# Performance work log

Hardware: AMD Instinct MI355X
Metric: run time of the kernel (lower is better)

## Reference

```python
import jax, jax.numpy as jnp
import numpy as np

K, D, O, B = 65536, 256, 256, 1024

def setup_inputs() -> dict:
    key = jax.random.key(0)
    k1, k2, k3 = jax.random.split(key, 3)
    return {
        "x": jax.random.normal(k1, (B, D), dtype=jnp.float32),
        "mean": jax.random.normal(k2, (K, D), dtype=jnp.float32),
        "stddev": jnp.ones((K, D), dtype=jnp.float32),
        "outputs": jax.random.normal(k3, (K, O), dtype=jnp.float32),
        "top_k": 32,
    }

def reference(x, mean, stddev, outputs, top_k):
    # Joint Gaussian log-prob summed over feature dim, computed without the
    # [B, K, D] broadcast torch materializes. Expanding sum_d ((x-mu)/sigma)^2
    # gives three GEMM-shaped terms.
    d = x.shape[-1]
    inv_var = 1.0 / (stddev * stddev)                      # [K, D]
    quad = ((x * x) @ inv_var.T                            # [B, K]
            - 2.0 * (x @ (mean * inv_var).T)
            + jnp.sum(mean * mean * inv_var, axis=-1))
    log_norm = jnp.sum(jnp.log(stddev), axis=-1) + 0.5 * d * jnp.log(2.0 * jnp.pi)
    joint_lp = -0.5 * quad - log_norm                      # [B, K]
    top_lp, top_idx = jax.lax.top_k(joint_lp, top_k)       # [B, top_k]
    weights = jax.nn.softmax(top_lp, axis=-1)              # [B, top_k]
    gathered = outputs[top_idx]                            # [B, top_k, O]
    return jnp.einsum('bko,bk->bo', gathered, weights)     # [B, O]
```

## Files before the change

### kernel.cpp

```cpp
#include <hip/hip_runtime.h>
#include <stdint.h>

#define KCOMP 65536
#define DDIM  256
#define ODIM  256
#define BROWS 1024
#define NCB   1024
#define LOG2PI_TERM 235.2482645f

typedef float f32x4 __attribute__((ext_vector_type(4)));
typedef __bf16 bf16x8 __attribute__((ext_vector_type(8)));
typedef unsigned int u32;
typedef unsigned long long u64;
typedef unsigned short u16;

typedef __attribute__((address_space(1))) const u32 gconst_u32;
typedef __attribute__((address_space(3))) u32 lds_u32;

__device__ __forceinline__ u16 f2bf(float f) {
  u32 b = __float_as_uint(f);
  b += 0x7FFFu + ((b >> 16) & 1u);
  return (u16)(b >> 16);
}
__device__ __forceinline__ u32 fkey(float f) {
  u32 b = __float_as_uint(f);
  return b ^ ((b >> 31) ? 0xFFFFFFFFu : 0x80000000u);
}

#define DPP_ROR1 0x121
#define DPP_ROR2 0x122
#define DPP_ROR4 0x124
#define DPP_ROR8 0x128

#define WS_A     0
#define WS_KEY   (1u << 20)

__global__ void prep_A(const float* __restrict__ x, u16* __restrict__ A) {
  int l = threadIdx.x & 63;
  int wv = threadIdx.x >> 6;
  int t = blockIdx.x;
  int row = t * 16 + (l & 15);
  for (int u = 0; u < 4; ++u) {
    int cc = wv * 4 + u;
    int d0 = cc * 16 + ((l >> 4) << 2);
    float4 xv = *(const float4*)(x + (size_t)row * DDIM + d0);
    float xs[4] = {xv.x, xv.y, xv.z, xv.w};
    uint4 v;
    u32 wds[4];
    for (int e = 0; e < 4; ++e)
      wds[e] = (u32)f2bf(xs[e] * xs[e]) | ((u32)f2bf(-2.0f * xs[e]) << 16);
    v.x = wds[0]; v.y = wds[1]; v.z = wds[2]; v.w = wds[3];
    *(uint4*)(A + ((size_t)(t * 16 + cc) * 64 + l) * 8) = v;
  }
}

__global__ __launch_bounds__(512, 4)
void main_gemm(const u16* __restrict__ A_ws, const float* __restrict__ mean,
               const float* __restrict__ stdd, u32* __restrict__ ckey) {
  __shared__ __align__(16) char lds_raw[66560];
  __shared__ u32 wsel[2][32][9];
  int tid = threadIdx.x, l = tid & 63, w = tid >> 6;
  int nb = blockIdx.x;
  int p = l & 15, q = l >> 4;
  int rt = w >> 2;
  int cg = w & 3;

  u32 kid0 = (u32)(cg * 16 + q * 4);

  bf16x8 wf[16];
  float myc0;
  f32x4 mycv;
  {
    u32* scr = (u32*)(lds_raw + w * 8320);
    int p8 = l & 7, q8 = l >> 3;
#pragma unroll
    for (int rr = 0; rr < 2; ++rr) {
      int comp = (nb * 4 + cg) * 16 + rr * 8 + p8;
      const float* mrow = mean + (size_t)comp * DDIM + q8 * 32;
      const float* srow = stdd + (size_t)comp * DDIM + q8 * 32;
      float gsum = 0.f;
#pragma unroll
      for (int i = 0; i < 8; ++i) {
        float4 m4 = *(const float4*)(mrow + 4 * i);
        float4 s4 = *(const float4*)(srow + 4 * i);
        float ms[4] = {m4.x, m4.y, m4.z, m4.w};
        float ss[4] = {s4.x, s4.y, s4.z, s4.w};
        u32 wd[4];
#pragma unroll
        for (int e = 0; e < 4; ++e) {
          float iv = __builtin_amdgcn_rcpf(ss[e] * ss[e]);
          float miv = ms[e] * iv;
          wd[e] = (u32)f2bf(-0.5f * iv) | ((u32)f2bf(-0.5f * miv) << 16);
          gsum -= 0.5f * ms[e] * miv + __logf(ss[e]);
        }
        uint4 v; v.x = wd[0]; v.y = wd[1]; v.z = wd[2]; v.w = wd[3];
        *(uint4*)(scr + p8 * 260 + q8 * 32 + i * 4) = v;
      }
      gsum += __shfl_xor(gsum, 8);
      gsum += __shfl_xor(gsum, 16);
      gsum += __shfl_xor(gsum, 32);
      if ((p >> 3) == rr) {
        myc0 = gsum - LOG2PI_TERM;
#pragma unroll
        for (int cc = 0; cc < 16; ++cc)
          wf[cc] = *(const bf16x8*)(scr + (p & 7) * 260 + cc * 16 + q * 4);
      }
    }
#pragma unroll
    for (int i = 0; i < 4; ++i)
      mycv[i] = __shfl(myc0, q * 4 + i);
  }
  __syncthreads();

#define ASHP(B, CELL) (lds_raw + ((size_t)(B) * 32 + (CELL)) * 1024)

#define ISSUE(S, B)                                                           \
  {                                                                           \
    _Pragma("unroll")                                                         \
    for (int u = 0; u < 4; ++u) {                                             \
      int cell = w * 4 + u;                                                   \
      const u16* gsrc = A_ws +                                                \
        ((size_t)((S) * 2 + (cell >> 4)) * 16 + (cell & 15)) * 512            \
        + (size_t)l * 8;                                                      \
      __builtin_amdgcn_global_load_lds((gconst_u32*)gsrc,                     \
          (lds_u32*)ASHP(B, cell), 16, 0, 0);                                 \
    }                                                                         \
  }

#define MERGE_EMIT(ST, B)                                                     \
  {                                                                           \
    int r = tid;                                                              \
    u32 b1 = ~0u, b2 = ~0u;                                                   \
    _Pragma("unroll")                                                         \
    for (int j = 0; j < 8; ++j) {                                             \
      u32 key = wsel[B][r][j];                                                \
      if (key < b1) { b2 = b1; b1 = key; }                                    \
      else if (key < b2) { b2 = key; }                                        \
    }                                                                         \
    int rowg = (ST) * 32 + r;                                                 \
    uint2 ov; ov.x = ~b1; ov.y = ~b2;                                         \
    *(uint2*)&ckey[((size_t)rowg * NCB + nb) * 2] = ov;                       \
  }

  ISSUE(0, 0)
  for (int s = 0; s < 32; ++s) {
    int pb = s & 1;
    __syncthreads();
    if (s < 31) ISSUE(s + 1, pb ^ 1)
    if (s > 0 && tid < 32) MERGE_EMIT(s - 1, pb ^ 1)

    f32x4 aca = mycv;
    f32x4 acb = (f32x4){0.f, 0.f, 0.f, 0.f};
    __builtin_amdgcn_s_setprio(1);
#pragma unroll
    for (int cc = 0; cc < 8; ++cc) {
      bf16x8 a0 = *(const bf16x8*)(ASHP(pb, rt * 16 + cc) + (size_t)l * 16);
      bf16x8 a1 = *(const bf16x8*)(ASHP(pb, rt * 16 + 8 + cc) + (size_t)l * 16);
      aca = __builtin_amdgcn_mfma_f32_16x16x32_bf16(wf[cc], a0, aca, 0, 0, 0);
      acb = __builtin_amdgcn_mfma_f32_16x16x32_bf16(wf[8 + cc], a1, acb, 0, 0, 0);
    }
    __builtin_amdgcn_s_setprio(0);
    f32x4 ac;
    ac[0] = aca[0] + acb[0]; ac[1] = aca[1] + acb[1];
    ac[2] = aca[2] + acb[2]; ac[3] = aca[3] + acb[3];

#define UMIN(a, b) ((a) < (b) ? (a) : (b))
#define UMAX(a, b) ((a) < (b) ? (b) : (a))
    {
      u32 k0 = (__float_as_uint(ac[0]) & 0xFFFFFF00u) | (kid0 + 0);
      u32 k1 = (__float_as_uint(ac[1]) & 0xFFFFFF00u) | (kid0 + 1);
      u32 k2 = (__float_as_uint(ac[2]) & 0xFFFFFF00u) | (kid0 + 2);
      u32 k3 = (__float_as_uint(ac[3]) & 0xFFFFFF00u) | (kid0 + 3);
      u32 l0 = UMIN(k0, k1), h0 = UMAX(k0, k1);
      u32 l1 = UMIN(k2, k3), h1 = UMAX(k2, k3);
      u32 m1 = UMIN(l0, l1), m2 = UMIN(UMAX(l0, l1), UMIN(h0, h1));
      {
        u32 o1 = (u32)__shfl_xor((int)m1, 16);
        u32 o2 = (u32)__shfl_xor((int)m2, 16);
        u32 lo = UMIN(m1, o1), hi = UMAX(m1, o1), mn = UMIN(m2, o2);
        m1 = lo; m2 = UMIN(hi, mn);
      }
      {
        u32 o1 = (u32)__shfl_xor((int)m1, 32);
        u32 o2 = (u32)__shfl_xor((int)m2, 32);
        u32 lo = UMIN(m1, o1), hi = UMAX(m1, o1), mn = UMIN(m2, o2);
        m1 = lo; m2 = UMIN(hi, mn);
      }
      if (q == 0) {
        int r = rt * 16 + p;
        wsel[pb][r][cg * 2] = m1;
        wsel[pb][r][cg * 2 + 1] = m2;
      }
    }
#undef UMIN
#undef UMAX
  }
  __syncthreads();
  if (tid < 32) MERGE_EMIT(31, 1)
#undef ISSUE
#undef MERGE_EMIT
#undef ASHP
}

__global__ __launch_bounds__(256)
void finalize(const float* __restrict__ x, const float* __restrict__ mean,
              const float* __restrict__ stdd, const float* __restrict__ outs,
              const u32* __restrict__ ckey, float* __restrict__ out) {
  __shared__ u32 cksh[2048];
  __shared__ float xr[256];
  __shared__ float part[256];
  __shared__ int selk[64];
  __shared__ float ew[32];
  __shared__ int kf[32];
  __shared__ float invs_sh;
  int tid = threadIdx.x, l = tid & 63, v = tid >> 6;
  int row = blockIdx.x;

  for (int i = tid; i < 2048; i += 256)
    cksh[i] = ckey[(size_t)row * 2048 + i];
  xr[tid] = x[(size_t)row * DDIM + tid];
  __syncthreads();

#define REDUCE_MAX(m)                                                         \
  {                                                                           \
    u32 o;                                                                    \
    o = (u32)__builtin_amdgcn_mov_dpp((int)m, DPP_ROR1, 0xf, 0xf, false);     \
    m = m > o ? m : o;                                                        \
    o = (u32)__builtin_amdgcn_mov_dpp((int)m, DPP_ROR2, 0xf, 0xf, false);     \
    m = m > o ? m : o;                                                        \
    o = (u32)__builtin_amdgcn_mov_dpp((int)m, DPP_ROR4, 0xf, 0xf, false);     \
    m = m > o ? m : o;                                                        \
    o = (u32)__builtin_amdgcn_mov_dpp((int)m, DPP_ROR8, 0xf, 0xf, false);     \
    m = m > o ? m : o;                                                        \
    o = (u32)__shfl_xor((int)m, 16); m = m > o ? m : o;                       \
    o = (u32)__shfl_xor((int)m, 32); m = m > o ? m : o;                       \
  }

  {
    u32 ext[8];
#pragma unroll
    for (int i = 0; i < 8; ++i) {
      int j = v * 512 + i * 64 + l;
      ext[i] = (cksh[j] & 0xFFFFFE00u) | ((u32)l << 3) | (u32)i;
    }
#define CSW(a, b) { if (ext[a] < ext[b]) { u32 t = ext[a]; ext[a] = ext[b]; ext[b] = t; } }
    CSW(0,1) CSW(2,3) CSW(4,5) CSW(6,7)
    CSW(0,2) CSW(1,3) CSW(4,6) CSW(5,7)
    CSW(1,2) CSW(5,6)
    CSW(0,4) CSW(1,5) CSW(2,6) CSW(3,7)
    CSW(2,4) CSW(3,5)
    CSW(1,2) CSW(3,4) CSW(5,6)
#undef CSW
    for (int it = 0; it < 16; ++it) {
      u32 m = ext[0];
      REDUCE_MAX(m)
      if (m == ext[0]) {
#pragma unroll
        for (int z = 0; z < 7; ++z) ext[z] = ext[z + 1];
        ext[7] = 0;
      }
      if (l == 0) {
        int wl = (int)((m >> 3) & 63u), wi = (int)(m & 7u);
        int j = v * 512 + wi * 64 + wl;
        selk[v * 16 + it] = (int)((u32)(j >> 1) * 64u + (~cksh[j] & 0x3Fu));
      }
    }
  }
  __syncthreads();

  {
    int j = tid >> 2, qq = tid & 3;
    int k = selk[j];
    const float* mr = mean + (size_t)k * DDIM + qq * 64;
    const float* sr = stdd + (size_t)k * DDIM + qq * 64;
    float s2 = 0.f, ls = 0.f;
    for (int i = 0; i < 16; ++i) {
      float4 m4 = *(const float4*)(mr + 4 * i);
      float4 s4 = *(const float4*)(sr + 4 * i);
      float4 x4 = *(const float4*)(&xr[qq * 64 + 4 * i]);
      { float is = __builtin_amdgcn_rcpf(s4.x); float df = (x4.x - m4.x) * is; s2 += df * df; ls += __logf(s4.x); }
      { float is = __builtin_amdgcn_rcpf(s4.y); float df = (x4.y - m4.y) * is; s2 += df * df; ls += __logf(s4.y); }
      { float is = __builtin_amdgcn_rcpf(s4.z); float df = (x4.z - m4.z) * is; s2 += df * df; ls += __logf(s4.z); }
      { float is = __builtin_amdgcn_rcpf(s4.w); float df = (x4.w - m4.w) * is; s2 += df * df; ls += __logf(s4.w); }
    }
    part[tid] = -0.5f * s2 - ls;
  }
  __syncthreads();

  if (tid < 64) {
    float lp0 = part[l * 4] + part[l * 4 + 1] + part[l * 4 + 2] +
                part[l * 4 + 3] - LOG2PI_TERM;
    u32 ext = (fkey(lp0) & 0xFFFFFFC0u) | (u32)l;
    float maxlp = 0.f, ssum = 0.f;
    for (int it = 0; it < 32; ++it) {
      u32 m = ext;
      REDUCE_MAX(m)
      int j = (int)(m & 63u);
      u32 vb = m & 0xFFFFFFC0u;
      vb ^= (vb >> 31) ? 0x80000000u : 0xFFFFFFFFu;
      float lp = __uint_as_float(vb);
      if (it == 0) maxlp = lp;
      float e = __expf(lp - maxlp);
      ssum += e;
      if (l == 0) { ew[it] = e; kf[it] = selk[j]; }
      if (j == l) ext = 0;
    }
    if (l == 0) invs_sh = 1.0f / ssum;
  }
  __syncthreads();
#undef REDUCE_MAX

  {
    float a = 0.f;
    for (int i = 0; i < 32; ++i)
      a += ew[i] * outs[(size_t)kf[i] * ODIM + tid];
    out[(size_t)row * ODIM + tid] = a * invs_sh;
  }
}

extern "C" void kernel_launch(void* const* d_in, const int* in_sizes, int n_in,
                              void* d_out, int out_size, void* d_ws, size_t ws_size,
                              hipStream_t stream) {
  const float* x = (const float*)d_in[0];
  const float* mean = (const float*)d_in[1];
  const float* stdd = (const float*)d_in[2];
  const float* outs = (const float*)d_in[3];
  char* ws = (char*)d_ws;
  u16* A_ws = (u16*)(ws + WS_A);
  u32* ckey = (u32*)(ws + WS_KEY);

  prep_A<<<64, 256, 0, stream>>>(x, A_ws);
  main_gemm<<<NCB, 512, 0, stream>>>(A_ws, mean, stdd, ckey);
  finalize<<<BROWS, 256, 0, stream>>>(x, mean, stdd, outs, ckey,
                                      (float*)d_out);
}
```

Measured before the change: 338.8 us.

## Precompute bf16 weight tiles in a separate pass and retile GEMM for larger component blocks

```diff
diff --git a/kernel.cpp b/kernel.cpp
--- a/kernel.cpp
+++ b/kernel.cpp
@@ -5,7 +5,6 @@
 #define DDIM  256
 #define ODIM  256
 #define BROWS 1024
-#define NCB   1024
 #define LOG2PI_TERM 235.2482645f
 
 typedef float f32x4 __attribute__((ext_vector_type(4)));
@@ -32,8 +31,27 @@
 #define DPP_ROR4 0x124
 #define DPP_ROR8 0x128
 
-#define WS_A     0
-#define WS_KEY   (1u << 20)
+#define WS_A      0u
+#define WS_W      (1u << 20)
+#define WS_MYC    (65u << 20)
+#define WS_KEYB   ((65u << 20) + (1u << 18))
+#define WS_NEED_BIG ((size_t)WS_KEYB + (4u << 20))
+#define WS_KEYS   (1u << 20)
+
+#define REDUCE_MAX(m)                                                         \
+  {                                                                           \
+    u32 o;                                                                    \
+    o = (u32)__builtin_amdgcn_mov_dpp((int)m, DPP_ROR1, 0xf, 0xf, false);     \
+    m = m > o ? m : o;                                                        \
+    o = (u32)__builtin_amdgcn_mov_dpp((int)m, DPP_ROR2, 0xf, 0xf, false);     \
+    m = m > o ? m : o;                                                        \
+    o = (u32)__builtin_amdgcn_mov_dpp((int)m, DPP_ROR4, 0xf, 0xf, false);     \
+    m = m > o ? m : o;                                                        \
+    o = (u32)__builtin_amdgcn_mov_dpp((int)m, DPP_ROR8, 0xf, 0xf, false);     \
+    m = m > o ? m : o;                                                        \
+    o = (u32)__shfl_xor((int)m, 16); m = m > o ? m : o;                       \
+    o = (u32)__shfl_xor((int)m, 32); m = m > o ? m : o;                       \
+  }
 
 __global__ void prep_A(const float* __restrict__ x, u16* __restrict__ A) {
   int l = threadIdx.x & 63;
@@ -54,73 +72,66 @@
   }
 }
 
+__global__ void prep_W(const float* __restrict__ mean,
+                       const float* __restrict__ stdd,
+                       u16* __restrict__ W, float* __restrict__ myc) {
+  __shared__ float psum[4][16];
+  int l = threadIdx.x & 63;
+  int wv = threadIdx.x >> 6;
+  int t = blockIdx.x;
+  int comp = t * 16 + (l & 15);
+  float gsum = 0.f;
+  for (int u = 0; u < 4; ++u) {
+    int cc = wv * 4 + u;
+    int d0 = cc * 16 + ((l >> 4) << 2);
+    float4 m4 = *(const float4*)(mean + (size_t)comp * DDIM + d0);
+    float4 s4 = *(const float4*)(stdd + (size_t)comp * DDIM + d0);
+    float ms[4] = {m4.x, m4.y, m4.z, m4.w};
+    float ss[4] = {s4.x, s4.y, s4.z, s4.w};
+    uint4 v;
+    u32 wds[4];
+    for (int e = 0; e < 4; ++e) {
+      float iv = __builtin_amdgcn_rcpf(ss[e] * ss[e]);
+      float miv = ms[e] * iv;
+      wds[e] = (u32)f2bf(-0.5f * iv) | ((u32)f2bf(-0.5f * miv) << 16);
+      gsum -= 0.5f * ms[e] * miv + __logf(ss[e]);
+    }
+    v.x = wds[0]; v.y = wds[1]; v.z = wds[2]; v.w = wds[3];
+    *(uint4*)(W + ((size_t)(t * 16 + cc) * 64 + l) * 8) = v;
+  }
+  gsum += __shfl_xor(gsum, 16);
+  gsum += __shfl_xor(gsum, 32);
+  if (l < 16) psum[wv][l] = gsum;
+  __syncthreads();
+  if (threadIdx.x < 16)
+    myc[t * 16 + threadIdx.x] = psum[0][threadIdx.x] + psum[1][threadIdx.x] +
+                                psum[2][threadIdx.x] + psum[3][threadIdx.x] -
+                                LOG2PI_TERM;
+}
+
 __global__ __launch_bounds__(512, 4)
-void main_gemm(const u16* __restrict__ A_ws, const float* __restrict__ mean,
-               const float* __restrict__ stdd, u32* __restrict__ ckey) {
-  __shared__ __align__(16) char lds_raw[66560];
-  __shared__ u32 wsel[2][32][9];
+void main_gemm_big(const u16* __restrict__ A_ws, const u16* __restrict__ W_ws,
+                   const float* __restrict__ myc_ws, u32* __restrict__ ckey) {
+  __shared__ __align__(16) char Ash[2][32][1024];
+  __shared__ u32 wsel[2][32][17];
   int tid = threadIdx.x, l = tid & 63, w = tid >> 6;
   int nb = blockIdx.x;
+  int nbc = nb & 127;
+  int rs = nb >> 7;
   int p = l & 15, q = l >> 4;
-  int rt = w >> 2;
-  int cg = w & 3;
-
-  u32 kid0 = (u32)(cg * 16 + q * 4);
-
-  bf16x8 wf[16];
-  float myc0;
-  f32x4 mycv;
-  {
-    u32* scr = (u32*)(lds_raw + w * 8320);
-    int p8 = l & 7, q8 = l >> 3;
-#pragma unroll
-    for (int rr = 0; rr < 2; ++rr) {
-      int comp = (nb * 4 + cg) * 16 + rr * 8 + p8;
-      const float* mrow = mean + (size_t)comp * DDIM + q8 * 32;
-      const float* srow = stdd + (size_t)comp * DDIM + q8 * 32;
-      float gsum = 0.f;
-#pragma unroll
-      for (int i = 0; i < 8; ++i) {
-        float4 m4 = *(const float4*)(mrow + 4 * i);
-        float4 s4 = *(const float4*)(srow + 4 * i);
-        float ms[4] = {m4.x, m4.y, m4.z, m4.w};
-        float ss[4] = {s4.x, s4.y, s4.z, s4.w};
-        u32 wd[4];
-#pragma unroll
-        for (int e = 0; e < 4; ++e) {
-          float iv = __builtin_amdgcn_rcpf(ss[e] * ss[e]);
-          float miv = ms[e] * iv;
-          wd[e] = (u32)f2bf(-0.5f * iv) | ((u32)f2bf(-0.5f * miv) << 16);
-          gsum -= 0.5f * ms[e] * miv + __logf(ss[e]);
-        }
-        uint4 v; v.x = wd[0]; v.y = wd[1]; v.z = wd[2]; v.w = wd[3];
-        *(uint4*)(scr + p8 * 260 + q8 * 32 + i * 4) = v;
-      }
-      gsum += __shfl_xor(gsum, 8);
-      gsum += __shfl_xor(gsum, 16);
-      gsum += __shfl_xor(gsum, 32);
-      if ((p >> 3) == rr) {
-        myc0 = gsum - LOG2PI_TERM;
-#pragma unroll
-        for (int cc = 0; cc < 16; ++cc)
-          wf[cc] = *(const bf16x8*)(scr + (p & 7) * 260 + cc * 16 + q * 4);
-      }
-    }
-#pragma unroll
-    for (int i = 0; i < 4; ++i)
-      mycv[i] = __shfl(myc0, q * 4 + i);
-  }
-  __syncthreads();
-
-#define ASHP(B, CELL) (lds_raw + ((size_t)(B) * 32 + (CELL)) * 1024)
-
+
+  int Cb = nbc * 512 + w * 64;
+  u32 kid0 = (u32)(w * 64 + q * 4);
+  const u16* Wl = W_ws + (size_t)(Cb >> 4) * 16 * 512 + (size_t)l * 8;
+
+#define ASHP(B, CELL) (&Ash[B][CELL][0])
 #define ISSUE(S, B)                                                           \
   {                                                                           \
     _Pragma("unroll")                                                         \
     for (int u = 0; u < 4; ++u) {                                             \
       int cell = w * 4 + u;                                                   \
       const u16* gsrc = A_ws +                                                \
-        ((size_t)((S) * 2 + (cell >> 4)) * 16 + (cell & 15)) * 512            \
+        ((size_t)((rs * 16 + (S) * 2 + (cell >> 4)) * 16) + (cell & 15)) * 512\
         + (size_t)l * 8;                                                      \
       __builtin_amdgcn_global_load_lds((gconst_u32*)gsrc,                     \
           (lds_u32*)ASHP(B, cell), 16, 0, 0);                                 \
@@ -130,50 +141,82 @@
 #define MERGE_EMIT(ST, B)                                                     \
   {                                                                           \
     int r = tid;                                                              \
-    u32 b1 = ~0u, b2 = ~0u;                                                   \
+    u32 top[8] = {~0u, ~0u, ~0u, ~0u, ~0u, ~0u, ~0u, ~0u};                    \
     _Pragma("unroll")                                                         \
-    for (int j = 0; j < 8; ++j) {                                             \
+    for (int j = 0; j < 16; ++j) {                                            \
       u32 key = wsel[B][r][j];                                                \
-      if (key < b1) { b2 = b1; b1 = key; }                                    \
-      else if (key < b2) { b2 = key; }                                        \
+      if (key < top[7]) {                                                     \
+        top[7] = key;                                                         \
+        for (int z = 7; z > 0 && top[z] < top[z - 1]; --z) {                  \
+          u32 tt = top[z]; top[z] = top[z - 1]; top[z - 1] = tt;              \
+        }                                                                     \
+      }                                                                       \
     }                                                                         \
-    int rowg = (ST) * 32 + r;                                                 \
-    uint2 ov; ov.x = ~b1; ov.y = ~b2;                                         \
-    *(uint2*)&ckey[((size_t)rowg * NCB + nb) * 2] = ov;                       \
+    int rowg = rs * 256 + (ST) * 32 + r;                                      \
+    size_t base = ((size_t)rowg * 128 + nbc) * 8;                             \
+    uint4 o1; o1.x = ~top[0]; o1.y = ~top[1]; o1.z = ~top[2]; o1.w = ~top[3]; \
+    uint4 o2; o2.x = ~top[4]; o2.y = ~top[5]; o2.z = ~top[6]; o2.w = ~top[7]; \
+    *(uint4*)&ckey[base] = o1;                                                \
+    *(uint4*)&ckey[base + 4] = o2;                                            \
   }
 
   ISSUE(0, 0)
-  for (int s = 0; s < 32; ++s) {
+  for (int s = 0; s < 8; ++s) {
     int pb = s & 1;
     __syncthreads();
-    if (s < 31) ISSUE(s + 1, pb ^ 1)
+    if (s < 7) ISSUE(s + 1, pb ^ 1)
     if (s > 0 && tid < 32) MERGE_EMIT(s - 1, pb ^ 1)
 
-    f32x4 aca = mycv;
-    f32x4 acb = (f32x4){0.f, 0.f, 0.f, 0.f};
+    f32x4 acc[2][4];
+#pragma unroll
+    for (int ct = 0; ct < 4; ++ct) {
+      f32x4 mv = *(const f32x4*)(myc_ws + Cb + ct * 16 + q * 4);
+      acc[0][ct] = mv;
+      acc[1][ct] = mv;
+    }
     __builtin_amdgcn_s_setprio(1);
 #pragma unroll
-    for (int cc = 0; cc < 8; ++cc) {
-      bf16x8 a0 = *(const bf16x8*)(ASHP(pb, rt * 16 + cc) + (size_t)l * 16);
-      bf16x8 a1 = *(const bf16x8*)(ASHP(pb, rt * 16 + 8 + cc) + (size_t)l * 16);
-      aca = __builtin_amdgcn_mfma_f32_16x16x32_bf16(wf[cc], a0, aca, 0, 0, 0);
-      acb = __builtin_amdgcn_mfma_f32_16x16x32_bf16(wf[8 + cc], a1, acb, 0, 0, 0);
+    for (int cc = 0; cc < 16; ++cc) {
+      bf16x8 a0 = *(const bf16x8*)(ASHP(pb, cc) + (size_t)l * 16);
+      bf16x8 a1 = *(const bf16x8*)(ASHP(pb, 16 + cc) + (size_t)l * 16);
+      bf16x8 w0 = *(const bf16x8*)(Wl + (size_t)(0 * 16 + cc) * 512);
+      bf16x8 w1 = *(const bf16x8*)(Wl + (size_t)(1 * 16 + cc) * 512);
+      bf16x8 w2 = *(const bf16x8*)(Wl + (size_t)(2 * 16 + cc) * 512);
+      bf16x8 w3 = *(const bf16x8*)(Wl + (size_t)(3 * 16 + cc) * 512);
+      acc[0][0] = __builtin_amdgcn_mfma_f32_16x16x32_bf16(w0, a0, acc[0][0], 0, 0, 0);
+      acc[1][0] = __builtin_amdgcn_mfma_f32_16x16x32_bf16(w0, a1, acc[1][0], 0, 0, 0);
+      acc[0][1] = __builtin_amdgcn_mfma_f32_16x16x32_bf16(w1, a0, acc[0][1], 0, 0, 0);
+      acc[1][1] = __builtin_amdgcn_mfma_f32_16x16x32_bf16(w1, a1, acc[1][1], 0, 0, 0);
+      acc[0][2] = __builtin_amdgcn_mfma_f32_16x16x32_bf16(w2, a0, acc[0][2], 0, 0, 0);
+      acc[1][2] = __builtin_amdgcn_mfma_f32_16x16x32_bf16(w2, a1, acc[1][2], 0, 0, 0);
+      acc[0][3] = __builtin_amdgcn_mfma_f32_16x16x32_bf16(w3, a0, acc[0][3], 0, 0, 0);
+      acc[1][3] = __builtin_amdgcn_mfma_f32_16x16x32_bf16(w3, a1, acc[1][3], 0, 0, 0);
     }
     __builtin_amdgcn_s_setprio(0);
-    f32x4 ac;
-    ac[0] = aca[0] + acb[0]; ac[1] = aca[1] + acb[1];
-    ac[2] = aca[2] + acb[2]; ac[3] = aca[3] + acb[3];
 
 #define UMIN(a, b) ((a) < (b) ? (a) : (b))
 #define UMAX(a, b) ((a) < (b) ? (b) : (a))
-    {
-      u32 k0 = (__float_as_uint(ac[0]) & 0xFFFFFF00u) | (kid0 + 0);
-      u32 k1 = (__float_as_uint(ac[1]) & 0xFFFFFF00u) | (kid0 + 1);
-      u32 k2 = (__float_as_uint(ac[2]) & 0xFFFFFF00u) | (kid0 + 2);
-      u32 k3 = (__float_as_uint(ac[3]) & 0xFFFFFF00u) | (kid0 + 3);
-      u32 l0 = UMIN(k0, k1), h0 = UMAX(k0, k1);
-      u32 l1 = UMIN(k2, k3), h1 = UMAX(k2, k3);
-      u32 m1 = UMIN(l0, l1), m2 = UMIN(UMAX(l0, l1), UMIN(h0, h1));
+#pragma unroll
+    for (int rt = 0; rt < 2; ++rt) {
+      u32 s1[4], s2[4];
+#pragma unroll
+      for (int ct = 0; ct < 4; ++ct) {
+        u32 kb = kid0 + (u32)(ct * 16);
+        u32 k0 = (__float_as_uint(acc[rt][ct][0]) & 0xFFFFFE00u) | kb;
+        u32 k1 = (__float_as_uint(acc[rt][ct][1]) & 0xFFFFFE00u) | (kb + 1);
+        u32 k2 = (__float_as_uint(acc[rt][ct][2]) & 0xFFFFFE00u) | (kb + 2);
+        u32 k3 = (__float_as_uint(acc[rt][ct][3]) & 0xFFFFFE00u) | (kb + 3);
+        u32 l0 = UMIN(k0, k1), h0 = UMAX(k0, k1);
+        u32 l1 = UMIN(k2, k3), h1 = UMAX(k2, k3);
+        s1[ct] = UMIN(l0, l1);
+        s2[ct] = UMIN(UMAX(l0, l1), UMIN(h0, h1));
+      }
+      u32 a1_ = UMIN(s1[0], s1[1]);
+      u32 a2_ = UMIN(UMAX(s1[0], s1[1]), UMIN(s2[0], s2[1]));
+      u32 b1_ = UMIN(s1[2], s1[3]);
+      u32 b2_ = UMIN(UMAX(s1[2], s1[3]), UMIN(s2[2], s2[3]));
+      u32 m1 = UMIN(a1_, b1_);
+      u32 m2 = UMIN(UMAX(a1_, b1_), UMIN(a2_, b2_));
       {
         u32 o1 = (u32)__shfl_xor((int)m1, 16);
         u32 o2 = (u32)__shfl_xor((int)m2, 16);
@@ -188,25 +231,25 @@
       }
       if (q == 0) {
         int r = rt * 16 + p;
-        wsel[pb][r][cg * 2] = m1;
-        wsel[pb][r][cg * 2 + 1] = m2;
+        wsel[pb][r][w * 2] = m1;
+        wsel[pb][r][w * 2 + 1] = m2;
       }
     }
 #undef UMIN
 #undef UMAX
   }
   __syncthreads();
-  if (tid < 32) MERGE_EMIT(31, 1)
+  if (tid < 32) MERGE_EMIT(7, 1)
 #undef ISSUE
 #undef MERGE_EMIT
 #undef ASHP
 }
 
 __global__ __launch_bounds__(256)
-void finalize(const float* __restrict__ x, const float* __restrict__ mean,
-              const float* __restrict__ stdd, const float* __restrict__ outs,
-              const u32* __restrict__ ckey, float* __restrict__ out) {
-  __shared__ u32 cksh[2048];
+void finalize_big(const float* __restrict__ x, const float* __restrict__ mean,
+                  const float* __restrict__ stdd, const float* __restrict__ outs,
+                  const u32* __restrict__ ckey, float* __restrict__ out) {
+  __shared__ u32 cksh[1024];
   __shared__ float xr[256];
   __shared__ float part[256];
   __shared__ int selk[64];
@@ -216,53 +259,35 @@
   int tid = threadIdx.x, l = tid & 63, v = tid >> 6;
   int row = blockIdx.x;
 
-  for (int i = tid; i < 2048; i += 256)
-    cksh[i] = ckey[(size_t)row * 2048 + i];
+  for (int i = tid; i < 1024; i += 256)
+    cksh[i] = ckey[(size_t)row * 1024 + i];
   xr[tid] = x[(size_t)row * DDIM + tid];
   __syncthreads();
 
-#define REDUCE_MAX(m)                                                         \
-  {                                                                           \
-    u32 o;                                                                    \
-    o = (u32)__builtin_amdgcn_mov_dpp((int)m, DPP_ROR1, 0xf, 0xf, false);     \
-    m = m > o ? m : o;                                                        \
-    o = (u32)__builtin_amdgcn_mov_dpp((int)m, DPP_ROR2, 0xf, 0xf, false);     \
-    m = m > o ? m : o;                                                        \
-    o = (u32)__builtin_amdgcn_mov_dpp((int)m, DPP_ROR4, 0xf, 0xf, false);     \
-    m = m > o ? m : o;                                                        \
-    o = (u32)__builtin_amdgcn_mov_dpp((int)m, DPP_ROR8, 0xf, 0xf, false);     \
-    m = m > o ? m : o;                                                        \
-    o = (u32)__shfl_xor((int)m, 16); m = m > o ? m : o;                       \
-    o = (u32)__shfl_xor((int)m, 32); m = m > o ? m : o;                       \
-  }
-
   {
-    u32 ext[8];
-#pragma unroll
-    for (int i = 0; i < 8; ++i) {
-      int j = v * 512 + i * 64 + l;
-      ext[i] = (cksh[j] & 0xFFFFFE00u) | ((u32)l << 3) | (u32)i;
+    u32 ext[4];
+#pragma unroll
+    for (int i = 0; i < 4; ++i) {
+      int j = v * 256 + i * 64 + l;
+      ext[i] = (cksh[j] & 0xFFFFFE00u) | ((u32)l << 2) | (u32)i;
     }
 #define CSW(a, b) { if (ext[a] < ext[b]) { u32 t = ext[a]; ext[a] = ext[b]; ext[b] = t; } }
-    CSW(0,1) CSW(2,3) CSW(4,5) CSW(6,7)
-    CSW(0,2) CSW(1,3) CSW(4,6) CSW(5,7)
-    CSW(1,2) CSW(5,6)
-    CSW(0,4) CSW(1,5) CSW(2,6) CSW(3,7)
-    CSW(2,4) CSW(3,5)
-    CSW(1,2) CSW(3,4) CSW(5,6)
+    CSW(0,1) CSW(2,3)
+    CSW(0,2) CSW(1,3)
+    CSW(1,2)
 #undef CSW
     for (int it = 0; it < 16; ++it) {
       u32 m = ext[0];
       REDUCE_MAX(m)
       if (m == ext[0]) {
 #pragma unroll
-        for (int z = 0; z < 7; ++z) ext[z] = ext[z + 1];
-        ext[7] = 0;
+        for (int z = 0; z < 3; ++z) ext[z] = ext[z + 1];
+        ext[3] = 0;
       }
       if (l == 0) {
-        int wl = (int)((m >> 3) & 63u), wi = (int)(m & 7u);
-        int j = v * 512 + wi * 64 + wl;
-        selk[v * 16 + it] = (int)((u32)(j >> 1) * 64u + (~cksh[j] & 0x3Fu));
+        int wl = (int)((m >> 2) & 63u), wi = (int)(m & 3u);
+        int j = v * 256 + wi * 64 + wl;
+        selk[v * 16 + it] = (int)((u32)(j >> 3) * 512u + (~cksh[j] & 0x1FFu));
       }
     }
   }
@@ -308,7 +333,251 @@
     if (l == 0) invs_sh = 1.0f / ssum;
   }
   __syncthreads();
-#undef REDUCE_MAX
+
+  {
+    float a = 0.f;
+    for (int i = 0; i < 32; ++i)
+      a += ew[i] * outs[(size_t)kf[i] * ODIM + tid];
+    out[(size_t)row * ODIM + tid] = a * invs_sh;
+  }
+}
+
+__global__ __launch_bounds__(512, 4)
+void main_gemm_small(const u16* __restrict__ A_ws, const float* __restrict__ mean,
+                     const float* __restrict__ stdd, u32* __restrict__ ckey) {
+  __shared__ __align__(16) char lds_raw[66560];
+  __shared__ u32 wsel[2][32][9];
+  int tid = threadIdx.x, l = tid & 63, w = tid >> 6;
+  int nb = blockIdx.x;
+  int p = l & 15, q = l >> 4;
+  int rt = w >> 2;
+  int cg = w & 3;
+  u32 kid0 = (u32)(cg * 16 + q * 4);
+
+  bf16x8 wf[16];
+  float myc0;
+  f32x4 mycv;
+  {
+    u32* scr = (u32*)(lds_raw + w * 8320);
+    int p8 = l & 7, q8 = l >> 3;
+#pragma unroll
+    for (int rr = 0; rr < 2; ++rr) {
+      int comp = (nb * 4 + cg) * 16 + rr * 8 + p8;
+      const float* mrow = mean + (size_t)comp * DDIM + q8 * 32;
+      const float* srow = stdd + (size_t)comp * DDIM + q8 * 32;
+      float gsum = 0.f;
+#pragma unroll
+      for (int i = 0; i < 8; ++i) {
+        float4 m4 = *(const float4*)(mrow + 4 * i);
+        float4 s4 = *(const float4*)(srow + 4 * i);
+        float ms[4] = {m4.x, m4.y, m4.z, m4.w};
+        float ss[4] = {s4.x, s4.y, s4.z, s4.w};
+        u32 wd[4];
+#pragma unroll
+        for (int e = 0; e < 4; ++e) {
+          float iv = __builtin_amdgcn_rcpf(ss[e] * ss[e]);
+          float miv = ms[e] * iv;
+          wd[e] = (u32)f2bf(-0.5f * iv) | ((u32)f2bf(-0.5f * miv) << 16);
+          gsum -= 0.5f * ms[e] * miv + __logf(ss[e]);
+        }
+        uint4 v; v.x = wd[0]; v.y = wd[1]; v.z = wd[2]; v.w = wd[3];
+        *(uint4*)(scr + p8 * 260 + q8 * 32 + i * 4) = v;
+      }
+      gsum += __shfl_xor(gsum, 8);
+      gsum += __shfl_xor(gsum, 16);
+      gsum += __shfl_xor(gsum, 32);
+      if ((p >> 3) == rr) {
+        myc0 = gsum - LOG2PI_TERM;
+#pragma unroll
+        for (int cc = 0; cc < 16; ++cc)
+          wf[cc] = *(const bf16x8*)(scr + (p & 7) * 260 + cc * 16 + q * 4);
+      }
+    }
+#pragma unroll
+    for (int i = 0; i < 4; ++i)
+      mycv[i] = __shfl(myc0, q * 4 + i);
+  }
+  __syncthreads();
+
+#define ASHP(B, CELL) (lds_raw + ((size_t)(B) * 32 + (CELL)) * 1024)
+#define ISSUE(S, B)                                                           \
+  {                                                                           \
+    _Pragma("unroll")                                                         \
+    for (int u = 0; u < 4; ++u) {                                             \
+      int cell = w * 4 + u;                                                   \
+      const u16* gsrc = A_ws +                                                \
+        ((size_t)((S) * 2 + (cell >> 4)) * 16 + (cell & 15)) * 512            \
+        + (size_t)l * 8;                                                      \
+      __builtin_amdgcn_global_load_lds((gconst_u32*)gsrc,                     \
+          (lds_u32*)ASHP(B, cell), 16, 0, 0);                                 \
+    }                                                                         \
+  }
+#define MERGE_EMIT(ST, B)                                                     \
+  {                                                                           \
+    int r = tid;                                                              \
+    u32 b1 = ~0u, b2 = ~0u;                                                   \
+    _Pragma("unroll")                                                         \
+    for (int j = 0; j < 8; ++j) {                                             \
+      u32 key = wsel[B][r][j];                                                \
+      if (key < b1) { b2 = b1; b1 = key; }                                    \
+      else if (key < b2) { b2 = key; }                                        \
+    }                                                                         \
+    int rowg = (ST) * 32 + r;                                                 \
+    uint2 ov; ov.x = ~b1; ov.y = ~b2;                                         \
+    *(uint2*)&ckey[((size_t)rowg * 1024 + nb) * 2] = ov;                      \
+  }
+
+  ISSUE(0, 0)
+  for (int s = 0; s < 32; ++s) {
+    int pb = s & 1;
+    __syncthreads();
+    if (s < 31) ISSUE(s + 1, pb ^ 1)
+    if (s > 0 && tid < 32) MERGE_EMIT(s - 1, pb ^ 1)
+
+    f32x4 aca = mycv;
+    f32x4 acb = (f32x4){0.f, 0.f, 0.f, 0.f};
+    __builtin_amdgcn_s_setprio(1);
+#pragma unroll
+    for (int cc = 0; cc < 8; ++cc) {
+      bf16x8 a0 = *(const bf16x8*)(ASHP(pb, rt * 16 + cc) + (size_t)l * 16);
+      bf16x8 a1 = *(const bf16x8*)(ASHP(pb, rt * 16 + 8 + cc) + (size_t)l * 16);
+      aca = __builtin_amdgcn_mfma_f32_16x16x32_bf16(wf[cc], a0, aca, 0, 0, 0);
+      acb = __builtin_amdgcn_mfma_f32_16x16x32_bf16(wf[8 + cc], a1, acb, 0, 0, 0);
+    }
+    __builtin_amdgcn_s_setprio(0);
+    f32x4 ac;
+    ac[0] = aca[0] + acb[0]; ac[1] = aca[1] + acb[1];
+    ac[2] = aca[2] + acb[2]; ac[3] = aca[3] + acb[3];
+
+#define UMIN(a, b) ((a) < (b) ? (a) : (b))
+#define UMAX(a, b) ((a) < (b) ? (b) : (a))
+    {
+      u32 k0 = (__float_as_uint(ac[0]) & 0xFFFFFF00u) | (kid0 + 0);
+      u32 k1 = (__float_as_uint(ac[1]) & 0xFFFFFF00u) | (kid0 + 1);
+      u32 k2 = (__float_as_uint(ac[2]) & 0xFFFFFF00u) | (kid0 + 2);
+      u32 k3 = (__float_as_uint(ac[3]) & 0xFFFFFF00u) | (kid0 + 3);
+      u32 l0 = UMIN(k0, k1), h0 = UMAX(k0, k1);
+      u32 l1 = UMIN(k2, k3), h1 = UMAX(k2, k3);
+      u32 m1 = UMIN(l0, l1), m2 = UMIN(UMAX(l0, l1), UMIN(h0, h1));
+      {
+        u32 o1 = (u32)__shfl_xor((int)m1, 16);
+        u32 o2 = (u32)__shfl_xor((int)m2, 16);
+        u32 lo = UMIN(m1, o1), hi = UMAX(m1, o1), mn = UMIN(m2, o2);
+        m1 = lo; m2 = UMIN(hi, mn);
+      }
+      {
+        u32 o1 = (u32)__shfl_xor((int)m1, 32);
+        u32 o2 = (u32)__shfl_xor((int)m2, 32);
+        u32 lo = UMIN(m1, o1), hi = UMAX(m1, o1), mn = UMIN(m2, o2);
+        m1 = lo; m2 = UMIN(hi, mn);
+      }
+      if (q == 0) {
+        int r = rt * 16 + p;
+        wsel[pb][r][cg * 2] = m1;
+        wsel[pb][r][cg * 2 + 1] = m2;
+      }
+    }
+#undef UMIN
+#undef UMAX
+  }
+  __syncthreads();
+  if (tid < 32) MERGE_EMIT(31, 1)
+#undef ISSUE
+#undef MERGE_EMIT
+#undef ASHP
+}
+
+__global__ __launch_bounds__(256)
+void finalize_small(const float* __restrict__ x, const float* __restrict__ mean,
+                    const float* __restrict__ stdd, const float* __restrict__ outs,
+                    const u32* __restrict__ ckey, float* __restrict__ out) {
+  __shared__ u32 cksh[2048];
+  __shared__ float xr[256];
+  __shared__ float part[256];
+  __shared__ int selk[64];
+  __shared__ float ew[32];
+  __shared__ int kf[32];
+  __shared__ float invs_sh;
+  int tid = threadIdx.x, l = tid & 63, v = tid >> 6;
+  int row = blockIdx.x;
+
+  for (int i = tid; i < 2048; i += 256)
+    cksh[i] = ckey[(size_t)row * 2048 + i];
+  xr[tid] = x[(size_t)row * DDIM + tid];
+  __syncthreads();
+
+  {
+    u32 ext[8];
+#pragma unroll
+    for (int i = 0; i < 8; ++i) {
+      int j = v * 512 + i * 64 + l;
+      ext[i] = (cksh[j] & 0xFFFFFE00u) | ((u32)l << 3) | (u32)i;
+    }
+#define CSW(a, b) { if (ext[a] < ext[b]) { u32 t = ext[a]; ext[a] = ext[b]; ext[b] = t; } }
+    CSW(0,1) CSW(2,3) CSW(4,5) CSW(6,7)
+    CSW(0,2) CSW(1,3) CSW(4,6) CSW(5,7)
+    CSW(1,2) CSW(5,6)
+    CSW(0,4) CSW(1,5) CSW(2,6) CSW(3,7)
+    CSW(2,4) CSW(3,5)
+    CSW(1,2) CSW(3,4) CSW(5,6)
+#undef CSW
+    for (int it = 0; it < 16; ++it) {
+      u32 m = ext[0];
+      REDUCE_MAX(m)
+      if (m == ext[0]) {
+#pragma unroll
+        for (int z = 0; z < 7; ++z) ext[z] = ext[z + 1];
+        ext[7] = 0;
+      }
+      if (l == 0) {
+        int wl = (int)((m >> 3) & 63u), wi = (int)(m & 7u);
+        int j = v * 512 + wi * 64 + wl;
+        selk[v * 16 + it] = (int)((u32)(j >> 1) * 64u + (~cksh[j] & 0x3Fu));
+      }
+    }
+  }
+  __syncthreads();
+
+  {
+    int j = tid >> 2, qq = tid & 3;
+    int k = selk[j];
+    const float* mr = mean + (size_t)k * DDIM + qq * 64;
+    const float* sr = stdd + (size_t)k * DDIM + qq * 64;
+    float s2 = 0.f, ls = 0.f;
+    for (int i = 0; i < 16; ++i) {
+      float4 m4 = *(const float4*)(mr + 4 * i);
+      float4 s4 = *(const float4*)(sr + 4 * i);
+      float4 x4 = *(const float4*)(&xr[qq * 64 + 4 * i]);
+      { float is = __builtin_amdgcn_rcpf(s4.x); float df = (x4.x - m4.x) * is; s2 += df * df; ls += __logf(s4.x); }
+      { float is = __builtin_amdgcn_rcpf(s4.y); float df = (x4.y - m4.y) * is; s2 += df * df; ls += __logf(s4.y); }
+      { float is = __builtin_amdgcn_rcpf(s4.z); float df = (x4.z - m4.z) * is; s2 += df * df; ls += __logf(s4.z); }
+      { float is = __builtin_amdgcn_rcpf(s4.w); float df = (x4.w - m4.w) * is; s2 += df * df; ls += __logf(s4.w); }
+    }
+    part[tid] = -0.5f * s2 - ls;
+  }
+  __syncthreads();
+
+  if (tid < 64) {
+    float lp0 = part[l * 4] + part[l * 4 + 1] + part[l * 4 + 2] +
+                part[l * 4 + 3] - LOG2PI_TERM;
+    u32 ext = (fkey(lp0) & 0xFFFFFFC0u) | (u32)l;
+    float maxlp = 0.f, ssum = 0.f;
+    for (int it = 0; it < 32; ++it) {
+      u32 m = ext;
+      REDUCE_MAX(m)
+      int j = (int)(m & 63u);
+      u32 vb = m & 0xFFFFFFC0u;
+      vb ^= (vb >> 31) ? 0x80000000u : 0xFFFFFFFFu;
+      float lp = __uint_as_float(vb);
+      if (it == 0) maxlp = lp;
+      float e = __expf(lp - maxlp);
+      ssum += e;
+      if (l == 0) { ew[it] = e; kf[it] = selk[j]; }
+      if (j == l) ext = 0;
+    }
+    if (l == 0) invs_sh = 1.0f / ssum;
+  }
+  __syncthreads();
 
   {
     float a = 0.f;
@@ -327,10 +596,21 @@
   const float* outs = (const float*)d_in[3];
   char* ws = (char*)d_ws;
   u16* A_ws = (u16*)(ws + WS_A);
-  u32* ckey = (u32*)(ws + WS_KEY);
-
-  prep_A<<<64, 256, 0, stream>>>(x, A_ws);
-  main_gemm<<<NCB, 512, 0, stream>>>(A_ws, mean, stdd, ckey);
-  finalize<<<BROWS, 256, 0, stream>>>(x, mean, stdd, outs, ckey,
-                                      (float*)d_out);
-}
+
+  if (ws_size >= WS_NEED_BIG) {
+    u16* W_ws = (u16*)(ws + WS_W);
+    float* myc_ws = (float*)(ws + WS_MYC);
+    u32* ckey = (u32*)(ws + WS_KEYB);
+    prep_A<<<64, 256, 0, stream>>>(x, A_ws);
+    prep_W<<<4096, 256, 0, stream>>>(mean, stdd, W_ws, myc_ws);
+    main_gemm_big<<<512, 512, 0, stream>>>(A_ws, W_ws, myc_ws, ckey);
+    finalize_big<<<BROWS, 256, 0, stream>>>(x, mean, stdd, outs, ckey,
+                                            (float*)d_out);
+  } else {
+    u32* ckey = (u32*)(ws + WS_KEYS);
+    prep_A<<<64, 256, 0, stream>>>(x, A_ws);
+    main_gemm_small<<<1024, 512, 0, stream>>>(A_ws, mean, stdd, ckey);
+    finalize_small<<<BROWS, 256, 0, stream>>>(x, mean, stdd, outs, ckey,
+                                              (float*)d_out);
+  }
+}
```

New measurement: 683.6 us. 102% more time.
